# Kernel optimization log

Hardware: AMD Instinct MI355X
Metric: run time of the kernel (lower is better)

## Reference

```python
import jax, jax.numpy as jnp
import numpy as np

NUM_ENT = 14541
NUM_REL = 474
D = 400
B = 32
N_CAND = 14505


def setup_inputs() -> dict:
    key = jax.random.key(0)
    k0, k1, k2, k4, k5 = jax.random.split(key, 5)
    return {
        "arg0_1": jax.random.normal(k0, (NUM_ENT, D), dtype=jnp.float32),   # entity embeddings
        "arg1_1": jax.random.normal(k1, (NUM_REL, D), dtype=jnp.float32),   # relation centers
        "arg2_1": jax.random.uniform(k2, (NUM_REL, D), dtype=jnp.float32),  # relation offsets (box widths)
        "arg3_1": jnp.ones((1,), dtype=jnp.float32),                        # margin gamma
        "arg4_1": jax.random.randint(k4, (B, 2), 0, NUM_REL),               # (head_id, rel_id) pairs
        "arg5_1": jax.random.randint(k5, (4, N_CAND), 0, NUM_ENT),          # candidate entity ids (row 0 used)
    }


def reference(arg0_1, arg1_1, arg2_1, arg3_1, arg4_1, arg5_1):
    # Gather heads / relation params
    head = arg0_1[arg4_1[:, 0]]            # [B, D]
    rel_c = arg1_1[arg4_1[:, 1]]           # [B, D]
    rel_o = arg2_1[arg4_1[:, 1]]           # [B, D]

    query = (head + rel_c)[:, None, :]     # [B, 1, D] box center
    offset = rel_o[:, None, :]             # [B, 1, D] box width

    # Candidate tail embeddings: only row 0 of arg5_1 is used in the graph
    cand = arg0_1[arg5_1[0].reshape(-1)][None, :, :]  # [1, N_CAND, D]

    d = jnp.abs(cand - query)                           # [B, N_CAND, D]
    dist_outside = jax.nn.relu(d - offset).sum(-1)      # [B, N_CAND]
    dist_inside = jnp.abs(jnp.minimum(d, offset)).sum(-1)

    return arg3_1 - dist_outside - 0.02 * dist_inside   # [B, N_CAND]
```

## Files before the change

### kernel.cpp

```cpp
#include <hip/hip_runtime.h>

#define DIM     400
#define NENT    14541
#define B       32
#define NCAND   14505
#define NROUND  3627
#define TSTRIPS 256
#define THREADS 256
#define CVTBLK  2841

typedef __attribute__((ext_vector_type(2))) _Float16 half2_t;

static __device__ __forceinline__ half2_t bch(unsigned u) {
    return __builtin_bit_cast(half2_t, u);
}
static __device__ __forceinline__ half2_t habs2(half2_t x) {
    unsigned u = __builtin_bit_cast(unsigned, x) & 0x7fff7fffu;
    return __builtin_bit_cast(half2_t, u);
}
static __device__ __forceinline__ unsigned pkh(float x, float y) {
    half2_t h;
    h.x = (_Float16)x;
    h.y = (_Float16)y;
    return __builtin_bit_cast(unsigned, h);
}
static __device__ __forceinline__ float dot2acc(half2_t m, float s) {
#if __has_builtin(__builtin_amdgcn_fdot2)
    const half2_t ones = {(_Float16)1.f, (_Float16)1.f};
    return __builtin_amdgcn_fdot2(m, ones, s, false);
#else
    return s + (float)m.x + (float)m.y;
#endif
}

__global__ void setup_kernel(const float* __restrict__ ent,
                             const float* __restrict__ relc,
                             const float* __restrict__ relo,
                             const float* __restrict__ onev,
                             const int*   __restrict__ pairs,
                             uint4* __restrict__ ent16,
                             _Float16* __restrict__ q16,
                             _Float16* __restrict__ o16,
                             float* __restrict__ baseg) {
    const int blk = blockIdx.x;
    const int tid = threadIdx.x;
    if (blk < CVTBLK) {
        const int TOT8 = NENT * DIM / 8;
        int i = blk * THREADS + tid;
        if (i >= TOT8) return;
        const float4* s4 = (const float4*)ent;
        float4 a = s4[2 * i], c = s4[2 * i + 1];
        uint4 d;
        d.x = pkh(a.x, a.y);
        d.y = pkh(a.z, a.w);
        d.z = pkh(c.x, c.y);
        d.w = pkh(c.z, c.w);
        ent16[i] = d;
    } else {
        const int b = blk - CVTBLK;
        const int h = pairs[2 * b + 0];
        const int r = pairs[2 * b + 1];
        float so = 0.f;
        for (int i = tid; i < DIM; i += THREADS) {
            float qv = ent[(size_t)h * DIM + i] + relc[(size_t)r * DIM + i];
            float ov = relo[(size_t)r * DIM + i];
            q16[(size_t)b * DIM + i] = (_Float16)qv;
            o16[(size_t)b * DIM + i] = (_Float16)(0.98f * ov);
            so += ov;
        }
        __shared__ float sred[4];
        for (int off = 32; off; off >>= 1) so += __shfl_down(so, off);
        if ((tid & 63) == 0) sred[tid >> 6] = so;
        __syncthreads();
        if (tid == 0)
            baseg[b] = onev[0] + 0.98f * (sred[0] + sred[1] + sred[2] + sred[3]);
    }
}

__global__ __launch_bounds__(THREADS, 2)
void score_f16(const uint4* __restrict__ ent16,
               const uint4* __restrict__ q16,
               const uint4* __restrict__ o16,
               const float* __restrict__ baseg,
               const int*   __restrict__ cidx,
               float* __restrict__ out) {
    const int fid  = blockIdx.x;
    const int xcd  = fid & 7;
    const int rest = fid >> 3;
    const int bq   = rest & 7;
    const int tc   = rest >> 3;
    const int t    = xcd + 8 * tc;

    const int tid  = threadIdx.x;
    const int lane = tid & 63;
    const int u    = lane & 15;
    const int g    = lane >> 4;
    const int b    = __builtin_amdgcn_readfirstlane(bq * 4 + (tid >> 6));

    const uint4* qb = q16 + (size_t)b * 50;
    const uint4* ob = o16 + (size_t)b * 50;
    uint4 qr0 = qb[u], qr1 = qb[u + 16], qr2 = qb[u + 32];
    uint4 or0 = ob[u], or1 = ob[u + 16], or2 = ob[u + 32];
    uint4 qr3 = qr0, or3 = or0;
    if (u < 2) { qr3 = qb[48 + u]; or3 = ob[48 + u]; }
    const float base = baseg[b];

    const half2_t K002 = {(_Float16)0.02f, (_Float16)0.02f};

#define PAIR(cu, qu, ou, SS)                                    \
    {                                                           \
        half2_t cc_ = bch(cu), qq_ = bch(qu), oo_ = bch(ou);    \
        half2_t dd_ = cc_ - qq_;                                \
        half2_t aa_ = habs2(dd_);                               \
        half2_t ee_ = aa_ * K002 + oo_;                         \
        half2_t mm_ = __builtin_elementwise_max(aa_, ee_);      \
        SS = dot2acc(mm_, SS);                                  \
    }
#define PROC(C, Q, O, SA, SB)                                   \
    PAIR(C.x, Q.x, O.x, SA) PAIR(C.y, Q.y, O.y, SB)             \
    PAIR(C.z, Q.z, O.z, SA) PAIR(C.w, Q.w, O.w, SB)

    for (int rr = t; rr < NROUND; rr += 2 * TSTRIPS) {
        const int rrB   = rr + TSTRIPS;
        const int candA = 4 * rr + g;
        const int candB = 4 * rrB + g;
        const int ciA = cidx[candA < NCAND ? candA : NCAND - 1];
        const int ciB = cidx[candB < NCAND ? candB : NCAND - 1];
        const uint4* pA = ent16 + (size_t)ciA * 50;
        const uint4* pB = ent16 + (size_t)ciB * 50;

        uint4 a0 = pA[u], a1 = pA[u + 16], a2 = pA[u + 32];
        uint4 b0 = pB[u], b1 = pB[u + 16], b2 = pB[u + 32];
        uint4 a3, b3;
        if (u < 2) { a3 = pA[48 + u]; b3 = pB[48 + u]; }

        float sa0 = 0.f, sa1 = 0.f, sb0 = 0.f, sb1 = 0.f;
        PROC(a0, qr0, or0, sa0, sa1)
        PROC(a1, qr1, or1, sa0, sa1)
        PROC(a2, qr2, or2, sa0, sa1)
        if (u < 2) { PROC(a3, qr3, or3, sa0, sa1) }
        PROC(b0, qr0, or0, sb0, sb1)
        PROC(b1, qr1, or1, sb0, sb1)
        PROC(b2, qr2, or2, sb0, sb1)
        if (u < 2) { PROC(b3, qr3, or3, sb0, sb1) }

        float sA = sa0 + sa1;
        float sB = sb0 + sb1;
        sA += __shfl_xor(sA, 1); sB += __shfl_xor(sB, 1);
        sA += __shfl_xor(sA, 2); sB += __shfl_xor(sB, 2);
        sA += __shfl_xor(sA, 4); sB += __shfl_xor(sB, 4);
        sA += __shfl_xor(sA, 8); sB += __shfl_xor(sB, 8);

        if (u == 0) {
            if (candA < NCAND) out[(size_t)b * NCAND + candA] = base - sA;
            if (candB < NCAND) out[(size_t)b * NCAND + candB] = base - sB;
        }
    }
#undef PROC
#undef PAIR
}

__global__ __launch_bounds__(THREADS, 2)
void score_f32(const float* __restrict__ ent,
               const float* __restrict__ relc,
               const float* __restrict__ relo,
               const float* __restrict__ onev,
               const int*   __restrict__ pairs,
               const int*   __restrict__ cidx,
               float* __restrict__ out) {
    const int fid  = blockIdx.x;
    const int xcd  = fid & 7;
    const int rest = fid >> 3;
    const int bq   = rest & 7;
    const int tc   = rest >> 3;
    const int t    = xcd + 8 * tc;

    const int tid  = threadIdx.x;
    const int lane = tid & 63;
    const int u    = lane & 15;
    const int g    = lane >> 4;
    const int b    = __builtin_amdgcn_readfirstlane(bq * 4 + (tid >> 6));

    const int hd = pairs[b * 2 + 0];
    const int rl = pairs[b * 2 + 1];
    const float4* hb = (const float4*)(ent  + (size_t)hd * DIM) + u;
    const float4* cb = (const float4*)(relc + (size_t)rl * DIM) + u;
    const float4* ob = (const float4*)(relo + (size_t)rl * DIM) + u;

    float4 q[7], o[7];
    float oa = 0.f;
#pragma unroll
    for (int k = 0; k < 6; ++k) {
        float4 h = hb[16 * k], c = cb[16 * k];
        q[k] = make_float4(h.x + c.x, h.y + c.y, h.z + c.z, h.w + c.w);
        o[k] = ob[16 * k];
        oa += o[k].x + o[k].y + o[k].z + o[k].w;
    }
    if (u < 4) {
        float4 h = hb[96], c = cb[96];
        q[6] = make_float4(h.x + c.x, h.y + c.y, h.z + c.z, h.w + c.w);
        o[6] = ob[96];
        oa += o[6].x + o[6].y + o[6].z + o[6].w;
    }
    oa += __shfl_xor(oa, 1);
    oa += __shfl_xor(oa, 2);
    oa += __shfl_xor(oa, 4);
    oa += __shfl_xor(oa, 8);
    const float base = onev[0] + 0.98f * oa;

    const float4* entu = (const float4*)ent + u;

#define E(vc, vq, vo, AM, AD)                     \
        {                                         \
            float d_ = (vc) - (vq);               \
            AM += fmaxf(fabsf(d_), (vo));         \
            AD += fabsf(d_);                      \
        }
#define F4(k, AM, AD)                             \
        E(cbuf[k].x, q[k].x, o[k].x, AM, AD)      \
        E(cbuf[k].y, q[k].y, o[k].y, AM, AD)      \
        E(cbuf[k].z, q[k].z, o[k].z, AM, AD)      \
        E(cbuf[k].w, q[k].w, o[k].w, AM, AD)

    for (int rr = t; rr < NROUND; rr += TSTRIPS) {
        const int cand = 4 * rr + g;
        const int ci   = cidx[cand < NCAND ? cand : NCAND - 1];
        const float4* p = entu + (size_t)ci * 100;

        float4 cbuf[7];
#pragma unroll
        for (int k = 0; k < 6; ++k) cbuf[k] = p[16 * k];
        if (u < 4) cbuf[6] = p[96];

        float am0 = 0.f, ad0 = 0.f, am1 = 0.f, ad1 = 0.f;
        F4(0, am0, ad0) F4(1, am1, ad1)
        F4(2, am0, ad0) F4(3, am1, ad1)
        F4(4, am0, ad0) F4(5, am1, ad1)
        if (u < 4) { F4(6, am0, ad0) }

        float s_ = fmaf(-0.98f, am0 + am1, -0.02f * (ad0 + ad1));
        s_ += __shfl_xor(s_, 1);
        s_ += __shfl_xor(s_, 2);
        s_ += __shfl_xor(s_, 4);
        s_ += __shfl_xor(s_, 8);

        if (u == 0 && cand < NCAND)
            out[(size_t)b * NCAND + cand] = base + s_;
    }
#undef F4
#undef E
}

extern "C" void kernel_launch(void* const* d_in, const int* in_sizes, int n_in,
                              void* d_out, int out_size, void* d_ws, size_t ws_size,
                              hipStream_t stream) {
    const float* ent   = (const float*)d_in[0];
    const float* relc  = (const float*)d_in[1];
    const float* relo  = (const float*)d_in[2];
    const float* onev  = (const float*)d_in[3];
    const int*   pairs = (const int*)d_in[4];
    const int*   cidx  = (const int*)d_in[5];
    float*       out   = (float*)d_out;

    const size_t entB = (size_t)NENT * DIM * 2;
    const size_t qB   = (size_t)B * DIM * 2;
    const size_t need = entB + 2 * qB + B * sizeof(float);
    const int grid = 8 * 8 * 32;

    if (ws_size >= need) {
        unsigned char* w = (unsigned char*)d_ws;
        uint4*    ent16 = (uint4*)w;
        _Float16* q16   = (_Float16*)(w + entB);
        _Float16* o16   = (_Float16*)(w + entB + qB);
        float*    baseg = (float*)(w + entB + 2 * qB);

        setup_kernel<<<CVTBLK + B, THREADS, 0, stream>>>(
            ent, relc, relo, onev, pairs, ent16, q16, o16, baseg);
        score_f16<<<grid, THREADS, 0, stream>>>(
            ent16, (const uint4*)q16, (const uint4*)o16, baseg, cidx, out);
    } else {
        score_f32<<<grid, THREADS, 0, stream>>>(ent, relc, relo, onev, pairs, cidx, out);
    }
}
```

Before: 41.82 us.

## Reuse each gathered candidate row across two batch queries per wave

```diff
diff --git a/kernel.cpp b/kernel.cpp
--- a/kernel.cpp
+++ b/kernel.cpp
@@ -87,23 +87,35 @@
     const int fid  = blockIdx.x;
     const int xcd  = fid & 7;
     const int rest = fid >> 3;
-    const int bq   = rest & 7;
-    const int tc   = rest >> 3;
+    const int beta = rest & 3;
+    const int tc   = rest >> 2;
     const int t    = xcd + 8 * tc;
 
     const int tid  = threadIdx.x;
+    const int wid  = tid >> 6;
     const int lane = tid & 63;
     const int u    = lane & 15;
     const int g    = lane >> 4;
-    const int b    = __builtin_amdgcn_readfirstlane(bq * 4 + (tid >> 6));
-
-    const uint4* qb = q16 + (size_t)b * 50;
-    const uint4* ob = o16 + (size_t)b * 50;
-    uint4 qr0 = qb[u], qr1 = qb[u + 16], qr2 = qb[u + 32];
-    uint4 or0 = ob[u], or1 = ob[u + 16], or2 = ob[u + 32];
-    uint4 qr3 = qr0, or3 = or0;
-    if (u < 2) { qr3 = qb[48 + u]; or3 = ob[48 + u]; }
-    const float base = baseg[b];
+    const int b0   = __builtin_amdgcn_readfirstlane(8 * beta + 2 * wid);
+    const int b1   = b0 + 1;
+
+    const uint4* qa = q16 + (size_t)b0 * 50;
+    const uint4* oa = o16 + (size_t)b0 * 50;
+    const uint4* qc = q16 + (size_t)b1 * 50;
+    const uint4* oc = o16 + (size_t)b1 * 50;
+
+    uint4 qA[4], oA[4], qB[4], oB[4];
+    qA[0] = qa[u]; qA[1] = qa[u + 16]; qA[2] = qa[u + 32];
+    oA[0] = oa[u]; oA[1] = oa[u + 16]; oA[2] = oa[u + 32];
+    qB[0] = qc[u]; qB[1] = qc[u + 16]; qB[2] = qc[u + 32];
+    oB[0] = oc[u]; oB[1] = oc[u + 16]; oB[2] = oc[u + 32];
+    qA[3] = qA[0]; oA[3] = oA[0]; qB[3] = qB[0]; oB[3] = oB[0];
+    if (u < 2) {
+        qA[3] = qa[48 + u]; oA[3] = oa[48 + u];
+        qB[3] = qc[48 + u]; oB[3] = oc[48 + u];
+    }
+    const float baseA = baseg[b0];
+    const float baseB = baseg[b1];
 
     const half2_t K002 = {(_Float16)0.02f, (_Float16)0.02f};
 
@@ -120,40 +132,37 @@
     PAIR(C.x, Q.x, O.x, SA) PAIR(C.y, Q.y, O.y, SB)             \
     PAIR(C.z, Q.z, O.z, SA) PAIR(C.w, Q.w, O.w, SB)
 
-    for (int rr = t; rr < NROUND; rr += 2 * TSTRIPS) {
-        const int rrB   = rr + TSTRIPS;
-        const int candA = 4 * rr + g;
-        const int candB = 4 * rrB + g;
-        const int ciA = cidx[candA < NCAND ? candA : NCAND - 1];
-        const int ciB = cidx[candB < NCAND ? candB : NCAND - 1];
-        const uint4* pA = ent16 + (size_t)ciA * 50;
-        const uint4* pB = ent16 + (size_t)ciB * 50;
-
-        uint4 a0 = pA[u], a1 = pA[u + 16], a2 = pA[u + 32];
-        uint4 b0 = pB[u], b1 = pB[u + 16], b2 = pB[u + 32];
-        uint4 a3, b3;
-        if (u < 2) { a3 = pA[48 + u]; b3 = pB[48 + u]; }
-
-        float sa0 = 0.f, sa1 = 0.f, sb0 = 0.f, sb1 = 0.f;
-        PROC(a0, qr0, or0, sa0, sa1)
-        PROC(a1, qr1, or1, sa0, sa1)
-        PROC(a2, qr2, or2, sa0, sa1)
-        if (u < 2) { PROC(a3, qr3, or3, sa0, sa1) }
-        PROC(b0, qr0, or0, sb0, sb1)
-        PROC(b1, qr1, or1, sb0, sb1)
-        PROC(b2, qr2, or2, sb0, sb1)
-        if (u < 2) { PROC(b3, qr3, or3, sb0, sb1) }
-
-        float sA = sa0 + sa1;
-        float sB = sb0 + sb1;
+    for (int rr = t; rr < NROUND; rr += TSTRIPS) {
+        const int cand = 4 * rr + g;
+        const int ci   = cidx[cand < NCAND ? cand : NCAND - 1];
+        const uint4* p = ent16 + (size_t)ci * 50;
+
+        uint4 cv0 = p[u], cv1 = p[u + 16], cv2 = p[u + 32];
+        uint4 cv3;
+        if (u < 2) cv3 = p[48 + u];
+
+        float sA0 = 0.f, sA1 = 0.f, sB0 = 0.f, sB1 = 0.f;
+        PROC(cv0, qA[0], oA[0], sA0, sA1)
+        PROC(cv1, qA[1], oA[1], sA0, sA1)
+        PROC(cv2, qA[2], oA[2], sA0, sA1)
+        PROC(cv0, qB[0], oB[0], sB0, sB1)
+        PROC(cv1, qB[1], oB[1], sB0, sB1)
+        PROC(cv2, qB[2], oB[2], sB0, sB1)
+        if (u < 2) {
+            PROC(cv3, qA[3], oA[3], sA0, sA1)
+            PROC(cv3, qB[3], oB[3], sB0, sB1)
+        }
+
+        float sA = sA0 + sA1;
+        float sB = sB0 + sB1;
         sA += __shfl_xor(sA, 1); sB += __shfl_xor(sB, 1);
         sA += __shfl_xor(sA, 2); sB += __shfl_xor(sB, 2);
         sA += __shfl_xor(sA, 4); sB += __shfl_xor(sB, 4);
         sA += __shfl_xor(sA, 8); sB += __shfl_xor(sB, 8);
 
-        if (u == 0) {
-            if (candA < NCAND) out[(size_t)b * NCAND + candA] = base - sA;
-            if (candB < NCAND) out[(size_t)b * NCAND + candB] = base - sB;
+        if (u == 0 && cand < NCAND) {
+            out[(size_t)b0 * NCAND + cand] = baseA - sA;
+            out[(size_t)b1 * NCAND + cand] = baseB - sB;
         }
     }
 #undef PROC
@@ -265,7 +274,6 @@
     const size_t entB = (size_t)NENT * DIM * 2;
     const size_t qB   = (size_t)B * DIM * 2;
     const size_t need = entB + 2 * qB + B * sizeof(float);
-    const int grid = 8 * 8 * 32;
 
     if (ws_size >= need) {
         unsigned char* w = (unsigned char*)d_ws;
@@ -276,9 +284,10 @@
 
         setup_kernel<<<CVTBLK + B, THREADS, 0, stream>>>(
             ent, relc, relo, onev, pairs, ent16, q16, o16, baseg);
-        score_f16<<<grid, THREADS, 0, stream>>>(
+        score_f16<<<8 * 4 * 32, THREADS, 0, stream>>>(
             ent16, (const uint4*)q16, (const uint4*)o16, baseg, cidx, out);
     } else {
-        score_f32<<<grid, THREADS, 0, stream>>>(ent, relc, relo, onev, pairs, cidx, out);
-    }
-}
+        score_f32<<<8 * 8 * 32, THREADS, 0, stream>>>(
+            ent, relc, relo, onev, pairs, cidx, out);
+    }
+}
```

Result: slower. 43.71 us (+4.5%).
